# Kernel tuning notes

Hardware: AMD Instinct MI355X
Metric: run time of the kernel (lower is better)

The kernel has to match this reference:

```python
import jax, jax.numpy as jnp
import numpy as np

N = 100000
E = 640000
C = 128
ALPHA = 0.1
BETA = 0.5
RESIDUAL = False


def setup_inputs() -> dict:
    key = jax.random.key(0)
    k1, k2, k3, k4, k5 = jax.random.split(key, 5)
    stdv = 1.0 / np.sqrt(C)
    x = jax.random.normal(k1, (N, C), dtype=jnp.float32)
    init_x = jax.random.normal(k2, (N, C), dtype=jnp.float32)
    weight = jax.random.uniform(k3, (C, C), dtype=jnp.float32, minval=-stdv, maxval=stdv)
    edge_index = jax.random.randint(k4, (2, E), 0, N, dtype=jnp.int64)
    edge_attr = jax.random.uniform(k5, (E,), dtype=jnp.float32)
    return {"x": x, "edge_index": edge_index, "edge_attr": edge_attr,
            "init_x": init_x, "weight": weight}


def reference(x, edge_index, edge_attr, init_x, weight):
    row, col = edge_index[0], edge_index[1]
    # spmm: out[row] += edge_attr * x[col]  (gather-scale-scatter)
    msgs = edge_attr[:, None] * x[col]                 # [E, C]
    hidden = jax.ops.segment_sum(msgs, row, num_segments=x.shape[0])  # [N, C]
    hidden = (1.0 - ALPHA) * hidden + ALPHA * init_x
    h = BETA * jnp.matmul(hidden, weight) + (1.0 - BETA) * hidden
    if RESIDUAL:
        h = h + x
    return h
```

## Files before the change

kernel.cpp:

```cpp
#include <hip/hip_runtime.h>


#define ALPHA 0.1f
#define BETA  0.5f
#define C_DIM 128
#define PAD   32
#define EB    4096
#define RB    512
#define WSCALE (32767.0f / 0.9f)
#define WDEC   (0.9f / 32767.0f)

typedef __attribute__((ext_vector_type(8))) short short8v;
typedef __attribute__((ext_vector_type(4))) float f32x4;

__device__ inline unsigned bf16rn(float f) {
    unsigned u = __float_as_uint(f);
    return (u + 0x7FFFu + ((u >> 16) & 1u)) >> 16;
}
__device__ inline unsigned pack2(float lo, float hi) {
    return bf16rn(lo) | (bf16rn(hi) << 16);
}

__global__ __launch_bounds__(256)
void k_part(const int* __restrict__ ei, const float* __restrict__ attr,
            const float4* __restrict__ x4, uint4* __restrict__ xb, int n8x,
            const float* __restrict__ W, ushort* __restrict__ Wt,
            uint2* __restrict__ slab, int* __restrict__ off,
            int E, int nbin, int nbuck) {
    int b = blockIdx.x;
    int t = threadIdx.x;
    if (b < nbin) {
        __shared__ int cnt_s[256];
        __shared__ int pre_s[256];
        cnt_s[t] = 0;
        __syncthreads();
        int e0 = b * EB;
        int eend = (e0 + EB < E) ? e0 + EB : E;
        for (int e = e0 + t; e < eend; e += 256)
            atomicAdd(&cnt_s[ei[e] >> 9], 1);
        __syncthreads();
        int v = cnt_s[t];
        pre_s[t] = v;
        for (int d = 1; d < 256; d <<= 1) {
            __syncthreads();
            int tmp = (t >= d) ? pre_s[t - d] : 0;
            __syncthreads();
            pre_s[t] += tmp;
        }
        __syncthreads();
        int excl = pre_s[t] - v;
        __syncthreads();
        pre_s[t] = excl;
        cnt_s[t] = 0;
        if (t < nbuck) off[b * (nbuck + 1) + t] = e0 + excl;
        if (t == 0)    off[b * (nbuck + 1) + nbuck] = eend;
        __syncthreads();
        for (int e = e0 + t; e < eend; e += 256) {
            int row = ei[e];
            int col = ei[E + e];
            float w = (1.0f - ALPHA) * attr[e];
            int wb = (int)(w * WSCALE + 0.5f);
            if (wb > 32767) wb = 32767;
            if (wb < 0) wb = 0;
            int bk = row >> 9;
            int rank = atomicAdd(&cnt_s[bk], 1);
            uint2 rec;
            rec.x = ((unsigned)col << 15) | (unsigned)wb;
            rec.y = (unsigned)row;
            slab[e0 + pre_s[bk] + rank] = rec;
        }
    } else {
        int i = (b - nbin) * 256 + t;
        if (i < n8x) {
            float4 a = x4[2 * i], c = x4[2 * i + 1];
            uint4 o;
            o.x = pack2(a.x, a.y); o.y = pack2(a.z, a.w);
            o.z = pack2(c.x, c.y); o.w = pack2(c.z, c.w);
            xb[i] = o;
        } else if (i < n8x + C_DIM * C_DIM) {
            int j = i - n8x;
            int n = j >> 7, k = j & 127;
            float v = BETA * W[k * C_DIM + n] + ((k == n) ? (1.0f - BETA) : 0.0f);
            Wt[j] = (ushort)bf16rn(v);
        }
    }
}

__global__ __launch_bounds__(256)
void k_ell(const uint2* __restrict__ slab, const int* __restrict__ off,
           int nbin, int nbuck, unsigned* __restrict__ recs,
           int* __restrict__ cnt, int N) {
    __shared__ int deg[RB];
    __shared__ unsigned ell[RB * PAD];
    int t = threadIdx.x;
    int beta = blockIdx.x;
    int r0 = beta * RB;
    for (int i = t; i < RB; i += 256) deg[i] = 0;
    __syncthreads();
    int wv = t >> 6, ln = t & 63;
    for (int s = wv; s < nbin; s += 4) {
        int st = off[s * (nbuck + 1) + beta];
        int en = off[s * (nbuck + 1) + beta + 1];
        for (int i = st + ln; i < en; i += 64) {
            uint2 rc = slab[i];
            int rl = (int)rc.y - r0;
            int rank = atomicAdd(&deg[rl], 1);
            if (rank < PAD) ell[rl * PAD + rank] = rc.x;
        }
    }
    __syncthreads();
    int nrows = N - r0;
    if (nrows > RB) nrows = RB;
    if (nrows <= 0) return;
    for (int i = t; i < nrows * PAD; i += 256)
        recs[(size_t)r0 * PAD + i] = ell[i];
    for (int i = t; i < nrows; i += 256) {
        int d = deg[i];
        cnt[r0 + i] = (d > PAD) ? PAD : d;
    }
}

__device__ inline void fma8(float* acc, float a, uint4 v) {
    acc[0] += a * __uint_as_float(v.x << 16);
    acc[1] += a * __uint_as_float(v.x & 0xffff0000u);
    acc[2] += a * __uint_as_float(v.y << 16);
    acc[3] += a * __uint_as_float(v.y & 0xffff0000u);
    acc[4] += a * __uint_as_float(v.z << 16);
    acc[5] += a * __uint_as_float(v.z & 0xffff0000u);
    acc[6] += a * __uint_as_float(v.w << 16);
    acc[7] += a * __uint_as_float(v.w & 0xffff0000u);
}

template <int MODE>
__global__ __launch_bounds__(256)
void k_gather(const void* __restrict__ xsrc, const float4* __restrict__ if4,
              const int* __restrict__ cnt, const unsigned* __restrict__ recs,
              uint4* __restrict__ hb, int N) {
    const int tid = threadIdx.x;
    long r = (long)blockIdx.x * 16 + (tid >> 4);
    if (r >= N) return;
    const int l = tid & 15;

    float4 iv0 = if4[r * 32 + 2 * l];
    float4 iv1 = if4[r * 32 + 2 * l + 1];
    int end = cnt[r];
    const uint4* rp = (const uint4*)(recs + (size_t)r * PAD);
    uint4 qa = rp[0];
    uint4 qb = rp[1];
    if (end > PAD) end = PAD;

    float acc[8];
    acc[0] = ALPHA * iv0.x; acc[1] = ALPHA * iv0.y;
    acc[2] = ALPHA * iv0.z; acc[3] = ALPHA * iv0.w;
    acc[4] = ALPHA * iv1.x; acc[5] = ALPHA * iv1.y;
    acc[6] = ALPHA * iv1.z; acc[7] = ALPHA * iv1.w;

    for (int k = 0; k < end; k += 8) {
        int   c0 = (int)(qa.x >> 15), c1 = (int)(qa.y >> 15);
        int   c2 = (int)(qa.z >> 15), c3 = (int)(qa.w >> 15);
        int   c4 = (int)(qb.x >> 15), c5 = (int)(qb.y >> 15);
        int   c6 = (int)(qb.z >> 15), c7 = (int)(qb.w >> 15);
        float w0 = (float)(qa.x & 0x7fffu) * WDEC;
        float w1 = (float)(qa.y & 0x7fffu) * WDEC;
        float w2 = (float)(qa.z & 0x7fffu) * WDEC;
        float w3 = (float)(qa.w & 0x7fffu) * WDEC;
        float w4 = (float)(qb.x & 0x7fffu) * WDEC;
        float w5 = (float)(qb.y & 0x7fffu) * WDEC;
        float w6 = (float)(qb.z & 0x7fffu) * WDEC;
        float w7 = (float)(qb.w & 0x7fffu) * WDEC;
        if (k + 1 >= end) { c1 = 0; w1 = 0.f; }
        if (k + 2 >= end) { c2 = 0; w2 = 0.f; }
        if (k + 3 >= end) { c3 = 0; w3 = 0.f; }
        if (k + 4 >= end) { c4 = 0; w4 = 0.f; }
        if (k + 5 >= end) { c5 = 0; w5 = 0.f; }
        if (k + 6 >= end) { c6 = 0; w6 = 0.f; }
        if (k + 7 >= end) { c7 = 0; w7 = 0.f; }
        bool more = (k + 8 < end);
        uint4 na, nb;
        if (more) { na = rp[(k >> 2) + 2]; nb = rp[(k >> 2) + 3]; }
        if (MODE == 1) {
            const uint4* xb4 = (const uint4*)xsrc;
            uint4 v0 = xb4[(size_t)c0 * 16 + l];
            uint4 v1 = xb4[(size_t)c1 * 16 + l];
            uint4 v2 = xb4[(size_t)c2 * 16 + l];
            uint4 v3 = xb4[(size_t)c3 * 16 + l];
            uint4 v4 = xb4[(size_t)c4 * 16 + l];
            uint4 v5 = xb4[(size_t)c5 * 16 + l];
            uint4 v6 = xb4[(size_t)c6 * 16 + l];
            uint4 v7 = xb4[(size_t)c7 * 16 + l];
            fma8(acc, w0, v0); fma8(acc, w1, v1);
            fma8(acc, w2, v2); fma8(acc, w3, v3);
            fma8(acc, w4, v4); fma8(acc, w5, v5);
            fma8(acc, w6, v6); fma8(acc, w7, v7);
        } else {
            const float4* x4 = (const float4*)xsrc;
            int cc[8] = {c0, c1, c2, c3, c4, c5, c6, c7};
            float ww[8] = {w0, w1, w2, w3, w4, w5, w6, w7};
#pragma unroll
            for (int j = 0; j < 8; ++j) {
                const float4* xr = x4 + (size_t)cc[j] * 32 + 2 * l;
                float4 a0 = xr[0], a1 = xr[1];
                float w = ww[j];
                acc[0] += w * a0.x; acc[1] += w * a0.y;
                acc[2] += w * a0.z; acc[3] += w * a0.w;
                acc[4] += w * a1.x; acc[5] += w * a1.y;
                acc[6] += w * a1.z; acc[7] += w * a1.w;
            }
        }
        if (more) { qa = na; qb = nb; }
    }
    uint4 o;
    o.x = pack2(acc[0], acc[1]);
    o.y = pack2(acc[2], acc[3]);
    o.z = pack2(acc[4], acc[5]);
    o.w = pack2(acc[6], acc[7]);
    hb[(size_t)r * 16 + l] = o;
}

__global__ __launch_bounds__(256)
void k_gemm(const uint4* __restrict__ hb, const ushort* __restrict__ Wt,
            float* __restrict__ out, int N) {
    const uint4* W16 = (const uint4*)Wt;
    int lane = threadIdx.x & 63;
    int wv   = threadIdx.x >> 6;
    int m = lane & 15, g = lane >> 4;
    long R0 = (long)blockIdx.x * 128 + wv * 32;

    long r[2];
#pragma unroll
    for (int t = 0; t < 2; ++t) {
        r[t] = R0 + t * 16 + m;
        if (r[t] >= N) r[t] = N - 1;
    }

    uint4 hv[2][4];
#pragma unroll
    for (int t = 0; t < 2; ++t)
#pragma unroll
        for (int ks = 0; ks < 4; ++ks)
            hv[t][ks] = hb[r[t] * 16 + ks * 4 + g];

    f32x4 acc[2][8];
#pragma unroll
    for (int t = 0; t < 2; ++t)
#pragma unroll
        for (int nt = 0; nt < 8; ++nt) acc[t][nt] = (f32x4){0.f, 0.f, 0.f, 0.f};

#pragma unroll
    for (int ks = 0; ks < 4; ++ks) {
        union { uint4 q; short8v s; } a0, a1;
        a0.q = hv[0][ks];
        a1.q = hv[1][ks];
#pragma unroll
        for (int nt = 0; nt < 8; ++nt) {
            union { uint4 q; short8v s; } b;
            b.q = W16[(nt * 16 + m) * 16 + (ks * 4 + g)];
            acc[0][nt] = __builtin_amdgcn_mfma_f32_16x16x32_bf16(a0.s, b.s, acc[0][nt], 0, 0, 0);
            acc[1][nt] = __builtin_amdgcn_mfma_f32_16x16x32_bf16(a1.s, b.s, acc[1][nt], 0, 0, 0);
        }
    }

#pragma unroll
    for (int t = 0; t < 2; ++t) {
        long rb = R0 + t * 16 + g * 4;
#pragma unroll
        for (int reg = 0; reg < 4; ++reg) {
            long rr = rb + reg;
            if (rr >= N) continue;
            float* outp = out + rr * C_DIM + m;
#pragma unroll
            for (int nt = 0; nt < 8; ++nt) outp[nt * 16] = acc[t][nt][reg];
        }
    }
}

extern "C" void kernel_launch(void* const* d_in, const int* in_sizes, int n_in,
                              void* d_out, int out_size, void* d_ws, size_t ws_size,
                              hipStream_t stream) {
    const float* x      = (const float*)d_in[0];
    const int*   ei     = (const int*)d_in[1];
    const float* attr   = (const float*)d_in[2];
    const float* init_x = (const float*)d_in[3];
    const float* W      = (const float*)d_in[4];
    float* out = (float*)d_out;

    const int N = in_sizes[0] / C_DIM;
    const int E = in_sizes[2];

    const int nbin  = (E + EB - 1) / EB;
    const int nbuck = (N + RB - 1) / RB;

    const int N_pad = (N + 255) & ~255;
    const size_t cnt_bytes  = (size_t)N_pad * 4;
    const size_t rec_bytes  = (size_t)nbuck * RB * PAD * 4;
    const size_t wt_bytes   = (size_t)C_DIM * C_DIM * 2;
    const size_t hb_bytes   = (size_t)N * C_DIM * 2;
    const size_t xb_bytes   = (size_t)N * C_DIM * 2;
    const size_t slab_bytes = (size_t)(nbin * EB) * 8;
    const size_t off_bytes  = (size_t)nbin * (nbuck + 1) * 4;
    const size_t hbr_bytes  = (hb_bytes > slab_bytes + off_bytes) ? hb_bytes
                                                                  : slab_bytes + off_bytes;
    const size_t base_need  = cnt_bytes + rec_bytes + wt_bytes + hbr_bytes;

    const int mode = (ws_size >= base_need + xb_bytes) ? 1 : 0;

    char* wsp = (char*)d_ws;
    int*      cnt  = (int*)wsp;
    unsigned* recs = (unsigned*)(wsp + cnt_bytes);
    ushort*   Wt   = (ushort*)((char*)recs + rec_bytes);
    char*     hbr  = (char*)Wt + wt_bytes;
    uint4*    hb   = (uint4*)hbr;
    uint2*    slab = (uint2*)hbr;
    int*      off  = (int*)(hbr + slab_bytes);
    uint4*    xb   = (mode == 1) ? (uint4*)(hbr + hbr_bytes) : nullptr;

    const int n8x = (mode == 1) ? (N * C_DIM / 8) : 0;
    const int nconv = (n8x + C_DIM * C_DIM + 255) / 256;

    k_part<<<nbin + nconv, 256, 0, stream>>>(ei, attr,
                                             (const float4*)x, xb, n8x,
                                             W, Wt, slab, off, E, nbin, nbuck);
    k_ell<<<nbuck, 256, 0, stream>>>(slab, off, nbin, nbuck, recs, cnt, N);

    if (mode == 1) {
        k_gather<1><<<(N + 15) / 16, 256, 0, stream>>>((const void*)xb, (const float4*)init_x,
                                                       cnt, recs, hb, N);
    } else {
        k_gather<0><<<(N + 15) / 16, 256, 0, stream>>>((const void*)x, (const float4*)init_x,
                                                       cnt, recs, hb, N);
    }
    k_gemm<<<(N + 127) / 128, 256, 0, stream>>>(hb, Wt, out, N);
}
```

Before: 115.7 us.

## Sort rows by degree within each bucket to balance gather work per wavefront

k_ell now builds a per-bucket degree histogram and prefix sum, then writes a permutation that groups rows of equal (capped) degree together. k_gather reads the permutation, so each wavefront processes rows with similar edge counts and spends fewer iterations idle on divergent loop trip counts. The cost is extra shared-memory atomics and syncs in k_ell, an added perm buffer and indirect load in the gather, and writes to hb rows that are no longer contiguous within a block.

Result: slower. 120.4 us (+4.1%).

```diff
diff --git a/kernel.cpp b/kernel.cpp
--- a/kernel.cpp
+++ b/kernel.cpp
@@ -89,9 +89,11 @@
 __global__ __launch_bounds__(256)
 void k_ell(const uint2* __restrict__ slab, const int* __restrict__ off,
            int nbin, int nbuck, unsigned* __restrict__ recs,
-           int* __restrict__ cnt, int N) {
+           int* __restrict__ cnt, int* __restrict__ perm, int N) {
     __shared__ int deg[RB];
     __shared__ unsigned ell[RB * PAD];
+    __shared__ int dh[PAD + 1];
+    __shared__ int dpre[PAD + 1];
     int t = threadIdx.x;
     int beta = blockIdx.x;
     int r0 = beta * RB;
@@ -114,9 +116,27 @@
     if (nrows <= 0) return;
     for (int i = t; i < nrows * PAD; i += 256)
         recs[(size_t)r0 * PAD + i] = ell[i];
+    if (t <= PAD) { dh[t] = 0; }
+    __syncthreads();
     for (int i = t; i < nrows; i += 256) {
         int d = deg[i];
-        cnt[r0 + i] = (d > PAD) ? PAD : d;
+        if (d > PAD) d = PAD;
+        cnt[r0 + i] = d;
+        atomicAdd(&dh[d], 1);
+    }
+    __syncthreads();
+    if (t == 0) {
+        int s = 0;
+        for (int d = 0; d <= PAD; ++d) { dpre[d] = s; s += dh[d]; }
+    }
+    __syncthreads();
+    if (t <= PAD) dh[t] = 0;
+    __syncthreads();
+    for (int i = t; i < nrows; i += 256) {
+        int d = deg[i];
+        if (d > PAD) d = PAD;
+        int rank = atomicAdd(&dh[d], 1);
+        perm[r0 + dpre[d] + rank] = r0 + i;
     }
 }
 
@@ -135,11 +155,12 @@
 __global__ __launch_bounds__(256)
 void k_gather(const void* __restrict__ xsrc, const float4* __restrict__ if4,
               const int* __restrict__ cnt, const unsigned* __restrict__ recs,
-              uint4* __restrict__ hb, int N) {
+              const int* __restrict__ perm, uint4* __restrict__ hb, int N) {
     const int tid = threadIdx.x;
-    long r = (long)blockIdx.x * 16 + (tid >> 4);
-    if (r >= N) return;
+    long vr = (long)blockIdx.x * 16 + (tid >> 4);
+    if (vr >= N) return;
     const int l = tid & 15;
+    long r = perm[vr];
 
     float4 iv0 = if4[r * 32 + 2 * l];
     float4 iv1 = if4[r * 32 + 2 * l + 1];
@@ -292,6 +313,7 @@
 
     const int N_pad = (N + 255) & ~255;
     const size_t cnt_bytes  = (size_t)N_pad * 4;
+    const size_t perm_bytes = (size_t)N_pad * 4;
     const size_t rec_bytes  = (size_t)nbuck * RB * PAD * 4;
     const size_t wt_bytes   = (size_t)C_DIM * C_DIM * 2;
     const size_t hb_bytes   = (size_t)N * C_DIM * 2;
@@ -300,13 +322,14 @@
     const size_t off_bytes  = (size_t)nbin * (nbuck + 1) * 4;
     const size_t hbr_bytes  = (hb_bytes > slab_bytes + off_bytes) ? hb_bytes
                                                                   : slab_bytes + off_bytes;
-    const size_t base_need  = cnt_bytes + rec_bytes + wt_bytes + hbr_bytes;
+    const size_t base_need  = cnt_bytes + perm_bytes + rec_bytes + wt_bytes + hbr_bytes;
 
     const int mode = (ws_size >= base_need + xb_bytes) ? 1 : 0;
 
     char* wsp = (char*)d_ws;
     int*      cnt  = (int*)wsp;
-    unsigned* recs = (unsigned*)(wsp + cnt_bytes);
+    int*      perm = (int*)(wsp + cnt_bytes);
+    unsigned* recs = (unsigned*)(wsp + cnt_bytes + perm_bytes);
     ushort*   Wt   = (ushort*)((char*)recs + rec_bytes);
     char*     hbr  = (char*)Wt + wt_bytes;
     uint4*    hb   = (uint4*)hbr;
@@ -320,14 +343,14 @@
     k_part<<<nbin + nconv, 256, 0, stream>>>(ei, attr,
                                              (const float4*)x, xb, n8x,
                                              W, Wt, slab, off, E, nbin, nbuck);
-    k_ell<<<nbuck, 256, 0, stream>>>(slab, off, nbin, nbuck, recs, cnt, N);
+    k_ell<<<nbuck, 256, 0, stream>>>(slab, off, nbin, nbuck, recs, cnt, perm, N);
 
     if (mode == 1) {
         k_gather<1><<<(N + 15) / 16, 256, 0, stream>>>((const void*)xb, (const float4*)init_x,
-                                                       cnt, recs, hb, N);
+                                                       cnt, recs, perm, hb, N);
     } else {
         k_gather<0><<<(N + 15) / 16, 256, 0, stream>>>((const void*)x, (const float4*)init_x,
-                                                       cnt, recs, hb, N);
+                                                       cnt, recs, perm, hb, N);
     }
     k_gemm<<<(N + 127) / 128, 256, 0, stream>>>(hb, Wt, out, N);
 }
```
